# Performance work log

Hardware: AMD Instinct MI355X
Metric: run time of the kernel (lower is better)

Reference implementation:

```python
import jax, jax.numpy as jnp
import numpy as np

K = 8192  # num_embeddings
COMMIT_WEIGHT = 0.25


def setup_inputs() -> dict:
    key = jax.random.key(0)
    k1, k2 = jax.random.split(key)
    B, T, D = 4, 2048, 512
    z = jax.random.normal(k1, (B, T, D), dtype=jnp.float32)
    padding_mask = jnp.zeros((B, T), dtype=bool)  # True = padded; all valid here
    # codebook init: normal(0, dim**-0.5)
    emb = jax.random.normal(k2, (K, D), dtype=jnp.float32) * (D ** -0.5)
    return {"z": z, "padding_mask": padding_mask, "emb": emb}


def reference(z, padding_mask, emb):
    B, T, D = z.shape
    flat = z.reshape(B * T, D)
    dist = (
        jnp.sum(flat * flat, axis=1, keepdims=True)
        - 2.0 * (flat @ emb.T)
        + jnp.sum(emb * emb, axis=1)[None, :]
    )
    indices = jnp.argmin(dist, axis=1)  # [B*T]
    z_q = emb[indices].reshape(B, T, D)
    z_residual = z - jax.lax.stop_gradient(z_q)

    valid = ~padding_mask  # [B, T], True = valid
    vmask = valid.astype(z.dtype)[..., None]  # [B, T, 1]
    n_valid = jnp.maximum(valid.sum(), 1)
    denom = (n_valid * D).astype(z.dtype)

    # commitment: mse(z, sg(z_q)); codebook: mse(z_q, sg(z)) over valid positions
    loss_commit = jnp.sum((z - jax.lax.stop_gradient(z_q)) ** 2 * vmask) / denom
    loss_codebook = jnp.sum((z_q - jax.lax.stop_gradient(z)) ** 2 * vmask) / denom
    vq_loss = loss_codebook + COMMIT_WEIGHT * loss_commit

    # batch stats over valid positions (detached scalars)
    w = valid.reshape(-1).astype(jnp.float32)
    counts = jnp.zeros((K,), dtype=jnp.float32).at[indices].add(w)
    total = jnp.maximum(counts.sum(), 1.0)
    p = counts / total
    entropy = -jnp.sum(p * jnp.log(p + 1e-10))
    perplexity = jnp.exp(entropy)
    codes_used = (counts > 0).sum().astype(jnp.float32)
    codes_used_frac = codes_used / float(K)

    return (z_residual, vq_loss, z_q, perplexity, codes_used, codes_used_frac)
```

## Files before the change

### kernel.cpp

```cpp
#include <hip/hip_runtime.h>
#include <math.h>


#define DDIM 512
#define MTOK 8192
#define KCODE 8192
#define NOUTE (MTOK * DDIM)

#define BM 128
#define BN 128
#define BK 32
#define NK (DDIM / BK)

#define OFF_EH 0u
#define OFF_EL (OFF_EH + (unsigned)KCODE * DDIM * 2u)
#define OFF_ZH (OFF_EL + (unsigned)KCODE * DDIM * 2u)
#define OFF_ZL (OFF_ZH + (unsigned)MTOK * DDIM * 2u)
#define OFF_EE (OFF_ZL + (unsigned)MTOK * DDIM * 2u)
#define OFF_ZZ (OFF_EE + KCODE * 4u)
#define OFF_PACKED (OFF_ZZ + MTOK * 4u)
#define OFF_COUNTS (OFF_PACKED + MTOK * 8u)
#define OFF_SSE (OFF_COUNTS + KCODE * 4u)

typedef _Float16 half8 __attribute__((ext_vector_type(8)));
typedef float f32x16 __attribute__((ext_vector_type(16)));

__global__ __launch_bounds__(256) void prep_kernel(const float* __restrict__ z,
                                                   const float* __restrict__ emb,
                                                   _Float16* __restrict__ eh,
                                                   _Float16* __restrict__ el,
                                                   _Float16* __restrict__ zh,
                                                   _Float16* __restrict__ zl,
                                                   float* __restrict__ zz,
                                                   float* __restrict__ ee) {
  const int row = blockIdx.x * 4 + (threadIdx.x >> 6);
  const int lane = threadIdx.x & 63;
  const float* src;
  _Float16 *dh, *dl;
  float* nrm;
  float sc;
  int r;
  if (row < KCODE) { src = emb + (size_t)row * DDIM; dh = eh; dl = el; nrm = ee; sc = 64.f; r = row; }
  else { src = z + (size_t)(row - KCODE) * DDIM; dh = zh; dl = zl; nrm = zz; sc = 1.f; r = row - KCODE; }
  const float4* s4 = reinterpret_cast<const float4*>(src);
  const float4 v0 = s4[lane * 2 + 0];
  const float4 v1 = s4[lane * 2 + 1];
  const float vv[8] = {v0.x, v0.y, v0.z, v0.w, v1.x, v1.y, v1.z, v1.w};
  half8 hv, lv;
  float s = 0.f;
#pragma unroll
  for (int i = 0; i < 8; ++i) {
    s = fmaf(vv[i], vv[i], s);
    const float vs = vv[i] * sc;
    const _Float16 h = (_Float16)vs;
    hv[i] = h;
    lv[i] = (_Float16)((vs - (float)h) * 2048.0f);
  }
  *reinterpret_cast<half8*>(dh + (size_t)r * DDIM + lane * 8) = hv;
  *reinterpret_cast<half8*>(dl + (size_t)r * DDIM + lane * 8) = lv;
#pragma unroll
  for (int off = 32; off > 0; off >>= 1) s += __shfl_down(s, off, 64);
  if (lane == 0) nrm[r] = s;
}

__device__ __forceinline__ void stage_tile(const char* gb, char* lb) {
#pragma unroll
  for (int i = 0; i < 8; ++i)
    __builtin_amdgcn_global_load_lds(
        (const __attribute__((address_space(1))) unsigned int*)(gb + i * 16384),
        (__attribute__((address_space(3))) unsigned int*)(lb + i * 1024), 16, 0, 0);
}

__global__ __launch_bounds__(256) void argmin_mfma_kernel(
    const _Float16* __restrict__ eh, const _Float16* __restrict__ el,
    const _Float16* __restrict__ zh, const _Float16* __restrict__ zl,
    const float* __restrict__ zz, const float* __restrict__ ee,
    unsigned long long* __restrict__ packed) {
  __shared__ __align__(16) unsigned char smem[65536];

  const int tid = threadIdx.x;
  const int l = tid & 63;
  const int w = tid >> 6;
  const int wr = w >> 1;
  const int wc = w & 1;
  const int codeBase = blockIdx.x * BM;
  const int tokBase = blockIdx.y * BN;

  const _Float16* tileSrc = (w == 0) ? eh + (size_t)codeBase * DDIM
                          : (w == 1) ? el + (size_t)codeBase * DDIM
                          : (w == 2) ? zh + (size_t)tokBase * DDIM
                                     : zl + (size_t)tokBase * DDIM;
  const int cS = (l & 3) ^ ((l >> 3) & 3);
  const char* gsrc = (const char*)tileSrc + (size_t)(l >> 2) * 1024 + cS * 16;
  char* ldsTile = (char*)smem + w * 8192;

  const int keyR = (l >> 1) & 3;
  const int rowA = wr * 64 + (l & 31);
  const int rowB = wc * 64 + (l & 31);
  const int aH = rowA * 64;
  const int aL = 8192 + rowA * 64;
  const int bH = 16384 + rowB * 64;
  const int bL = 24576 + rowB * 64;

  f32x16 hh[2][2], xx[2][2];
#pragma unroll
  for (int mt = 0; mt < 2; ++mt)
#pragma unroll
    for (int nt = 0; nt < 2; ++nt)
#pragma unroll
      for (int i = 0; i < 16; ++i) { hh[mt][nt][i] = 0.f; xx[mt][nt][i] = 0.f; }

#define LDF(off) (*(const half8*)((const char*)smem + (off)))
#define MFMA(a, b, c) __builtin_amdgcn_mfma_f32_32x32x16_f16((a), (b), (c), 0, 0, 0)

  stage_tile(gsrc, ldsTile);
  asm volatile("s_waitcnt vmcnt(0)" ::: "memory");
  __syncthreads();

#pragma unroll 1
  for (int c = 0; c < NK; ++c) {
    const int cur = c & 1;
    if (c + 1 < NK)
      stage_tile(gsrc + (size_t)(c + 1) * 64, ldsTile + (cur ^ 1) * 32768);
    const int bo = cur * 32768;
#pragma unroll
    for (int ks = 0; ks < 2; ++ks) {
      const int cs = ((ks * 2 + (l >> 5)) ^ keyR) << 4;
      const half8 a0h = LDF(bo + aH + cs);
      const half8 a1h = LDF(bo + aH + 2048 + cs);
      const half8 a0l = LDF(bo + aL + cs);
      const half8 a1l = LDF(bo + aL + 2048 + cs);
      const half8 b0h = LDF(bo + bH + cs);
      const half8 b1h = LDF(bo + bH + 2048 + cs);
      const half8 b0l = LDF(bo + bL + cs);
      const half8 b1l = LDF(bo + bL + 2048 + cs);
      hh[0][0] = MFMA(a0h, b0h, hh[0][0]);
      hh[0][1] = MFMA(a0h, b1h, hh[0][1]);
      hh[1][0] = MFMA(a1h, b0h, hh[1][0]);
      hh[1][1] = MFMA(a1h, b1h, hh[1][1]);
      xx[0][0] = MFMA(a0h, b0l, xx[0][0]);
      xx[0][1] = MFMA(a0h, b1l, xx[0][1]);
      xx[1][0] = MFMA(a1h, b0l, xx[1][0]);
      xx[1][1] = MFMA(a1h, b1l, xx[1][1]);
      xx[0][0] = MFMA(a0l, b0h, xx[0][0]);
      xx[0][1] = MFMA(a0l, b1h, xx[0][1]);
      xx[1][0] = MFMA(a1l, b0h, xx[1][0]);
      xx[1][1] = MFMA(a1l, b1h, xx[1][1]);
    }
    asm volatile("s_waitcnt vmcnt(0)" ::: "memory");
    __syncthreads();
  }

  float* eeS = (float*)smem;
  float* pd = (float*)(smem + 512);
  int* pi = (int*)(smem + 1536);
  if (tid < BM) eeS[tid] = ee[codeBase + tid];
  __syncthreads();
#pragma unroll
  for (int nt = 0; nt < 2; ++nt) {
    const int lt = wc * 64 + nt * 32 + (l & 31);
    const float ztt = zz[tokBase + lt];
    float bd = INFINITY;
    int bi = 0x7fffffff;
#pragma unroll
    for (int mt = 0; mt < 2; ++mt)
#pragma unroll
      for (int r = 0; r < 16; ++r) {
        const int rowL = wr * 64 + mt * 32 + (r & 3) + ((r >> 2) << 3) + ((l >> 5) << 2);
        const float dot = hh[mt][nt][r] * (1.0f / 64.0f) + xx[mt][nt][r] * (1.0f / 131072.0f);
        const float dist = (ztt - 2.0f * dot) + eeS[rowL];
        const int code = codeBase + rowL;
        if (dist < bd || (dist == bd && code < bi)) { bd = dist; bi = code; }
      }
    const float od = __shfl_xor(bd, 32, 64);
    const int oi = __shfl_xor(bi, 32, 64);
    if (od < bd || (od == bd && oi < bi)) { bd = od; bi = oi; }
    if (l < 32) { pd[w * 64 + nt * 32 + l] = bd; pi[w * 64 + nt * 32 + l] = bi; }
  }
  __syncthreads();
  if (tid < BN) {
    const int wcc = tid >> 6, rest = tid & 63;
    float da = pd[wcc * 64 + rest];
    int ia = pi[wcc * 64 + rest];
    const float db = pd[(2 + wcc) * 64 + rest];
    const int ib = pi[(2 + wcc) * 64 + rest];
    if (db < da || (db == da && ib < ia)) { da = db; ia = ib; }
    unsigned fb = __float_as_uint(da);
    fb ^= ((unsigned)((int)fb >> 31)) | 0x80000000u;
    const unsigned long long key = ((unsigned long long)fb << 32) | (unsigned)ia;
    atomicMin(&packed[tokBase + tid], key);
  }
#undef LDF
#undef MFMA
}

__global__ __launch_bounds__(256) void gather_kernel(const float* __restrict__ z,
                                                     const float* __restrict__ emb,
                                                     const unsigned long long* __restrict__ packed,
                                                     const unsigned char* __restrict__ mask,
                                                     float* __restrict__ out,
                                                     float* __restrict__ counts,
                                                     double* __restrict__ sse) {
  const int t = blockIdx.x * 4 + (threadIdx.x >> 6);
  const int lane = threadIdx.x & 63;
  const int idx = (int)(packed[t] & 0xffffffffull);
  const float* zp = z + (size_t)t * DDIM;
  const float* ep = emb + (size_t)idx * DDIM;
  float* rp = out + (size_t)t * DDIM;
  float* qp = out + (size_t)NOUTE + 1 + (size_t)t * DDIM;
  float s = 0.f;
#pragma unroll
  for (int j = 0; j < 8; ++j) {
    const int d = j * 64 + lane;
    const float zv = zp[d];
    const float ev = ep[d];
    const float r = zv - ev;
    rp[d] = r;
    qp[d] = ev;
    s = fmaf(r, r, s);
  }
#pragma unroll
  for (int off = 32; off > 0; off >>= 1) s += __shfl_down(s, off, 64);
  if (lane == 0) {
    const float wgt = mask[t] ? 0.0f : 1.0f;
    atomicAdd(sse, (double)s * (double)wgt);
    atomicAdd(&counts[idx], wgt);
  }
}

__global__ __launch_bounds__(1024) void stats_kernel(const float* __restrict__ counts,
                                                     const unsigned char* __restrict__ mask,
                                                     const double* __restrict__ sse,
                                                     float* __restrict__ out) {
  __shared__ double sd[1024];
  __shared__ int si[1024];
  const int tid = threadIdx.x;

  int nv = 0;
  for (int i = tid; i < MTOK; i += 1024) nv += (mask[i] ? 0 : 1);
  si[tid] = nv;
  __syncthreads();
#pragma unroll
  for (int s = 512; s > 0; s >>= 1) {
    if (tid < s) si[tid] += si[tid + s];
    __syncthreads();
  }
  const int n_valid = si[0];
  __syncthreads();

  double ct = 0.0;
  for (int k = tid; k < KCODE; k += 1024) ct += (double)counts[k];
  sd[tid] = ct;
  __syncthreads();
#pragma unroll
  for (int s = 512; s > 0; s >>= 1) {
    if (tid < s) sd[tid] += sd[tid + s];
    __syncthreads();
  }
  const float total = fmaxf((float)sd[0], 1.0f);
  __syncthreads();

  double ent = 0.0;
  int used = 0;
  for (int k = tid; k < KCODE; k += 1024) {
    const float c = counts[k];
    if (c > 0.f) ++used;
    const float p = c / total;
    ent += (double)(p * logf(p + 1e-10f));
  }
  sd[tid] = ent;
  si[tid] = used;
  __syncthreads();
#pragma unroll
  for (int s = 512; s > 0; s >>= 1) {
    if (tid < s) { sd[tid] += sd[tid + s]; si[tid] += si[tid + s]; }
    __syncthreads();
  }
  if (tid == 0) {
    const float entropy = -(float)sd[0];
    const float perp = expf(entropy);
    const int usedc = si[0];
    const int nv1 = n_valid > 1 ? n_valid : 1;
    const float denom = (float)(nv1 * DDIM);
    const float L = (float)sse[0] / denom;
    out[NOUTE] = L + 0.25f * L;
    out[2 * NOUTE + 1] = perp;
    out[2 * NOUTE + 2] = (float)usedc;
    out[2 * NOUTE + 3] = (float)usedc / (float)KCODE;
  }
}

extern "C" void kernel_launch(void* const* d_in, const int* in_sizes, int n_in,
                              void* d_out, int out_size, void* d_ws, size_t ws_size,
                              hipStream_t stream) {
  const float* z = (const float*)d_in[0];
  const unsigned char* mask = (const unsigned char*)d_in[1];
  const float* emb = (const float*)d_in[2];
  float* out = (float*)d_out;
  char* ws = (char*)d_ws;

  _Float16* eh = (_Float16*)(ws + OFF_EH);
  _Float16* el = (_Float16*)(ws + OFF_EL);
  _Float16* zh = (_Float16*)(ws + OFF_ZH);
  _Float16* zl = (_Float16*)(ws + OFF_ZL);
  float* ee = (float*)(ws + OFF_EE);
  float* zz = (float*)(ws + OFF_ZZ);
  unsigned long long* packed = (unsigned long long*)(ws + OFF_PACKED);
  float* counts = (float*)(ws + OFF_COUNTS);
  double* sse = (double*)(ws + OFF_SSE);

  hipMemsetAsync(ws + OFF_PACKED, 0xFF, MTOK * 8u, stream);
  hipMemsetAsync(ws + OFF_COUNTS, 0, KCODE * 4u + 8u, stream);

  hipLaunchKernelGGL(prep_kernel, dim3((KCODE + MTOK) / 4), dim3(256), 0, stream,
                     z, emb, eh, el, zh, zl, zz, ee);
  hipLaunchKernelGGL(argmin_mfma_kernel, dim3(KCODE / BM, MTOK / BN), dim3(256), 0, stream,
                     eh, el, zh, zl, zz, ee, packed);
  hipLaunchKernelGGL(gather_kernel, dim3(MTOK / 4), dim3(256), 0, stream,
                     z, emb, packed, mask, out, counts, sse);
  hipLaunchKernelGGL(stats_kernel, dim3(1), dim3(1024), 0, stream,
                     counts, mask, sse, out);
}
```

Baseline: 436.4 us.

## Replace split-fp16 distance GEMM with single fp16 pass plus bounded fp32 rescue

Drops the hi/lo fp16 split, so the argmin GEMM runs one fp16 MFMA product instead of three and staging traffic is halved. To stay exact, each tile records every code whose approximate distance falls within an error bound (built from the norms) of the running minimum. A new rescue kernel then recomputes those candidates in fp32 and picks the true argmin before gathering. If a token overflows its 128-slot candidate list it falls back to a full fp32 scan over all codes. The cost is extra atomics, candidate writes and per-token fp32 dot products.

After: 597.1 us. +36.8%, slower.

```diff
diff --git a/kernel.cpp b/kernel.cpp
--- a/kernel.cpp
+++ b/kernel.cpp
@@ -11,72 +11,90 @@
 #define BN 128
 #define BK 32
 #define NK (DDIM / BK)
+#define NCAND 128
+#define MARGIN_SLACK 0.02f
 
 #define OFF_EH 0u
-#define OFF_EL (OFF_EH + (unsigned)KCODE * DDIM * 2u)
-#define OFF_ZH (OFF_EL + (unsigned)KCODE * DDIM * 2u)
-#define OFF_ZL (OFF_ZH + (unsigned)MTOK * DDIM * 2u)
-#define OFF_EE (OFF_ZL + (unsigned)MTOK * DDIM * 2u)
+#define OFF_ZH (OFF_EH + (unsigned)KCODE * DDIM * 2u)
+#define OFF_EE (OFF_ZH + (unsigned)MTOK * DDIM * 2u)
 #define OFF_ZZ (OFF_EE + KCODE * 4u)
-#define OFF_PACKED (OFF_ZZ + MTOK * 4u)
-#define OFF_COUNTS (OFF_PACKED + MTOK * 8u)
+#define OFF_SEE (OFF_ZZ + MTOK * 4u)
+#define OFF_SZZ (OFF_SEE + KCODE * 4u)
+#define OFF_PACKED (OFF_SZZ + MTOK * 4u)
+#define OFF_CAND (OFF_PACKED + MTOK * 8u)
+#define OFF_CCNT (OFF_CAND + (unsigned)MTOK * NCAND * 8u)
+#define OFF_COUNTS (OFF_CCNT + MTOK * 4u)
 #define OFF_SSE (OFF_COUNTS + KCODE * 4u)
+#define OFF_SEMAX (OFF_SSE + 8u)
+#define ZERO_BYTES (MTOK * 4u + KCODE * 4u + 8u + 4u)
 
 typedef _Float16 half8 __attribute__((ext_vector_type(8)));
 typedef float f32x16 __attribute__((ext_vector_type(16)));
+
+__device__ __forceinline__ unsigned enc_f(float x) {
+  unsigned u = __float_as_uint(x);
+  return u ^ (((unsigned)((int)u >> 31)) | 0x80000000u);
+}
+__device__ __forceinline__ float dec_f(unsigned y) {
+  return __uint_as_float((y & 0x80000000u) ? (y ^ 0x80000000u) : ~y);
+}
 
 __global__ __launch_bounds__(256) void prep_kernel(const float* __restrict__ z,
                                                    const float* __restrict__ emb,
                                                    _Float16* __restrict__ eh,
-                                                   _Float16* __restrict__ el,
                                                    _Float16* __restrict__ zh,
-                                                   _Float16* __restrict__ zl,
                                                    float* __restrict__ zz,
-                                                   float* __restrict__ ee) {
+                                                   float* __restrict__ ee,
+                                                   float* __restrict__ see,
+                                                   float* __restrict__ szz,
+                                                   unsigned* __restrict__ semax) {
   const int row = blockIdx.x * 4 + (threadIdx.x >> 6);
   const int lane = threadIdx.x & 63;
   const float* src;
-  _Float16 *dh, *dl;
-  float* nrm;
-  float sc;
+  _Float16* dh;
+  float *nrm, *sq;
   int r;
-  if (row < KCODE) { src = emb + (size_t)row * DDIM; dh = eh; dl = el; nrm = ee; sc = 64.f; r = row; }
-  else { src = z + (size_t)(row - KCODE) * DDIM; dh = zh; dl = zl; nrm = zz; sc = 1.f; r = row - KCODE; }
+  bool isEmb;
+  if (row < KCODE) { src = emb + (size_t)row * DDIM; dh = eh; nrm = ee; sq = see; r = row; isEmb = true; }
+  else { src = z + (size_t)(row - KCODE) * DDIM; dh = zh; nrm = zz; sq = szz; r = row - KCODE; isEmb = false; }
   const float4* s4 = reinterpret_cast<const float4*>(src);
   const float4 v0 = s4[lane * 2 + 0];
   const float4 v1 = s4[lane * 2 + 1];
   const float vv[8] = {v0.x, v0.y, v0.z, v0.w, v1.x, v1.y, v1.z, v1.w};
-  half8 hv, lv;
+  half8 hv;
   float s = 0.f;
 #pragma unroll
   for (int i = 0; i < 8; ++i) {
     s = fmaf(vv[i], vv[i], s);
-    const float vs = vv[i] * sc;
-    const _Float16 h = (_Float16)vs;
-    hv[i] = h;
-    lv[i] = (_Float16)((vs - (float)h) * 2048.0f);
+    hv[i] = (_Float16)vv[i];
   }
   *reinterpret_cast<half8*>(dh + (size_t)r * DDIM + lane * 8) = hv;
-  *reinterpret_cast<half8*>(dl + (size_t)r * DDIM + lane * 8) = lv;
 #pragma unroll
   for (int off = 32; off > 0; off >>= 1) s += __shfl_down(s, off, 64);
-  if (lane == 0) nrm[r] = s;
-}
-
-__device__ __forceinline__ void stage_tile(const char* gb, char* lb) {
-#pragma unroll
-  for (int i = 0; i < 8; ++i)
+  if (lane == 0) {
+    nrm[r] = s;
+    const float q = sqrtf(s);
+    sq[r] = q;
+    if (isEmb) atomicMax(semax, enc_f(q));
+  }
+}
+
+__device__ __forceinline__ void stage_half(const char* gb, char* lb) {
+#pragma unroll
+  for (int i = 0; i < 4; ++i)
     __builtin_amdgcn_global_load_lds(
         (const __attribute__((address_space(1))) unsigned int*)(gb + i * 16384),
         (__attribute__((address_space(3))) unsigned int*)(lb + i * 1024), 16, 0, 0);
 }
 
 __global__ __launch_bounds__(256) void argmin_mfma_kernel(
-    const _Float16* __restrict__ eh, const _Float16* __restrict__ el,
-    const _Float16* __restrict__ zh, const _Float16* __restrict__ zl,
+    const _Float16* __restrict__ eh, const _Float16* __restrict__ zh,
     const float* __restrict__ zz, const float* __restrict__ ee,
-    unsigned long long* __restrict__ packed) {
-  __shared__ __align__(16) unsigned char smem[65536];
+    const float* __restrict__ see, const float* __restrict__ szz,
+    const unsigned* __restrict__ semaxp,
+    unsigned long long* __restrict__ packed,
+    int* __restrict__ ccnt, unsigned long long* __restrict__ cand) {
+  __shared__ __align__(16) unsigned char smem[32768];
 
   const int tid = threadIdx.x;
   const int l = tid & 63;
@@ -86,34 +104,30 @@
   const int codeBase = blockIdx.x * BM;
   const int tokBase = blockIdx.y * BN;
 
-  const _Float16* tileSrc = (w == 0) ? eh + (size_t)codeBase * DDIM
-                          : (w == 1) ? el + (size_t)codeBase * DDIM
-                          : (w == 2) ? zh + (size_t)tokBase * DDIM
-                                     : zl + (size_t)tokBase * DDIM;
+  const _Float16* tileSrc = (w < 2) ? eh + (size_t)codeBase * DDIM
+                                    : zh + (size_t)tokBase * DDIM;
   const int cS = (l & 3) ^ ((l >> 3) & 3);
-  const char* gsrc = (const char*)tileSrc + (size_t)(l >> 2) * 1024 + cS * 16;
-  char* ldsTile = (char*)smem + w * 8192;
+  const char* gsrc = (const char*)tileSrc + (size_t)((w & 1) * 64 + (l >> 2)) * 1024 + cS * 16;
+  char* ldsHalf = (char*)smem + (w >> 1) * 8192 + (w & 1) * 4096;
 
   const int keyR = (l >> 1) & 3;
   const int rowA = wr * 64 + (l & 31);
   const int rowB = wc * 64 + (l & 31);
   const int aH = rowA * 64;
-  const int aL = 8192 + rowA * 64;
-  const int bH = 16384 + rowB * 64;
-  const int bL = 24576 + rowB * 64;
-
-  f32x16 hh[2][2], xx[2][2];
+  const int bH = 8192 + rowB * 64;
+
+  f32x16 hh[2][2];
 #pragma unroll
   for (int mt = 0; mt < 2; ++mt)
 #pragma unroll
     for (int nt = 0; nt < 2; ++nt)
 #pragma unroll
-      for (int i = 0; i < 16; ++i) { hh[mt][nt][i] = 0.f; xx[mt][nt][i] = 0.f; }
+      for (int i = 0; i < 16; ++i) hh[mt][nt][i] = 0.f;
 
 #define LDF(off) (*(const half8*)((const char*)smem + (off)))
 #define MFMA(a, b, c) __builtin_amdgcn_mfma_f32_32x32x16_f16((a), (b), (c), 0, 0, 0)
 
-  stage_tile(gsrc, ldsTile);
+  stage_half(gsrc, ldsHalf);
   asm volatile("s_waitcnt vmcnt(0)" ::: "memory");
   __syncthreads();
 
@@ -121,45 +135,38 @@
   for (int c = 0; c < NK; ++c) {
     const int cur = c & 1;
     if (c + 1 < NK)
-      stage_tile(gsrc + (size_t)(c + 1) * 64, ldsTile + (cur ^ 1) * 32768);
-    const int bo = cur * 32768;
+      stage_half(gsrc + (size_t)(c + 1) * 64, ldsHalf + (cur ^ 1) * 16384);
+    const int bo = cur * 16384;
 #pragma unroll
     for (int ks = 0; ks < 2; ++ks) {
       const int cs = ((ks * 2 + (l >> 5)) ^ keyR) << 4;
-      const half8 a0h = LDF(bo + aH + cs);
-      const half8 a1h = LDF(bo + aH + 2048 + cs);
-      const half8 a0l = LDF(bo + aL + cs);
-      const half8 a1l = LDF(bo + aL + 2048 + cs);
-      const half8 b0h = LDF(bo + bH + cs);
-      const half8 b1h = LDF(bo + bH + 2048 + cs);
-      const half8 b0l = LDF(bo + bL + cs);
-      const half8 b1l = LDF(bo + bL + 2048 + cs);
-      hh[0][0] = MFMA(a0h, b0h, hh[0][0]);
-      hh[0][1] = MFMA(a0h, b1h, hh[0][1]);
-      hh[1][0] = MFMA(a1h, b0h, hh[1][0]);
-      hh[1][1] = MFMA(a1h, b1h, hh[1][1]);
-      xx[0][0] = MFMA(a0h, b0l, xx[0][0]);
-      xx[0][1] = MFMA(a0h, b1l, xx[0][1]);
-      xx[1][0] = MFMA(a1h, b0l, xx[1][0]);
-      xx[1][1] = MFMA(a1h, b1l, xx[1][1]);
-      xx[0][0] = MFMA(a0l, b0h, xx[0][0]);
-      xx[0][1] = MFMA(a0l, b1h, xx[0][1]);
-      xx[1][0] = MFMA(a1l, b0h, xx[1][0]);
-      xx[1][1] = MFMA(a1l, b1h, xx[1][1]);
+      const half8 a0 = LDF(bo + aH + cs);
+      const half8 a1 = LDF(bo + aH + 2048 + cs);
+      const half8 b0 = LDF(bo + bH + cs);
+      const half8 b1 = LDF(bo + bH + 2048 + cs);
+      hh[0][0] = MFMA(a0, b0, hh[0][0]);
+      hh[0][1] = MFMA(a0, b1, hh[0][1]);
+      hh[1][0] = MFMA(a1, b0, hh[1][0]);
+      hh[1][1] = MFMA(a1, b1, hh[1][1]);
     }
     asm volatile("s_waitcnt vmcnt(0)" ::: "memory");
     __syncthreads();
   }
 
   float* eeS = (float*)smem;
-  float* pd = (float*)(smem + 512);
-  int* pi = (int*)(smem + 1536);
-  if (tid < BM) eeS[tid] = ee[codeBase + tid];
-  __syncthreads();
+  float* seeS = (float*)(smem + 512);
+  float* pd = (float*)(smem + 1024);
+  int* pi = (int*)(smem + 2048);
+  float* lim = (float*)(smem + 3072);
+  if (tid < BM) { eeS[tid] = ee[codeBase + tid]; seeS[tid] = see[codeBase + tid]; }
+  __syncthreads();
+
+  float ztt[2], szt[2];
 #pragma unroll
   for (int nt = 0; nt < 2; ++nt) {
     const int lt = wc * 64 + nt * 32 + (l & 31);
-    const float ztt = zz[tokBase + lt];
+    ztt[nt] = zz[tokBase + lt];
+    szt[nt] = szz[tokBase + lt];
     float bd = INFINITY;
     int bi = 0x7fffffff;
 #pragma unroll
@@ -167,8 +174,7 @@
 #pragma unroll
       for (int r = 0; r < 16; ++r) {
         const int rowL = wr * 64 + mt * 32 + (r & 3) + ((r >> 2) << 3) + ((l >> 5) << 2);
-        const float dot = hh[mt][nt][r] * (1.0f / 64.0f) + xx[mt][nt][r] * (1.0f / 131072.0f);
-        const float dist = (ztt - 2.0f * dot) + eeS[rowL];
+        const float dist = (ztt[nt] - 2.0f * hh[mt][nt][r]) + eeS[rowL];
         const int code = codeBase + rowL;
         if (dist < bd || (dist == bd && code < bi)) { bd = dist; bi = code; }
       }
@@ -185,46 +191,121 @@
     const float db = pd[(2 + wcc) * 64 + rest];
     const int ib = pi[(2 + wcc) * 64 + rest];
     if (db < da || (db == da && ib < ia)) { da = db; ia = ib; }
-    unsigned fb = __float_as_uint(da);
-    fb ^= ((unsigned)((int)fb >> 31)) | 0x80000000u;
-    const unsigned long long key = ((unsigned long long)fb << 32) | (unsigned)ia;
+    const unsigned long long key = ((unsigned long long)enc_f(da) << 32) | (unsigned)ia;
     atomicMin(&packed[tokBase + tid], key);
+    const unsigned long long curk = packed[tokBase + tid];
+    lim[tid] = fminf(da, dec_f((unsigned)(curk >> 32)));
+  }
+  __syncthreads();
+
+  const float semaxv = dec_f(*semaxp);
+#pragma unroll
+  for (int nt = 0; nt < 2; ++nt) {
+    const int lt = wc * 64 + nt * 32 + (l & 31);
+    const float L = lim[lt];
+    const int tokG = tokBase + lt;
+#pragma unroll
+    for (int mt = 0; mt < 2; ++mt)
+#pragma unroll
+      for (int r = 0; r < 16; ++r) {
+        const int rowL = wr * 64 + mt * 32 + (r & 3) + ((r >> 2) << 3) + ((l >> 5) << 2);
+        const float dist = (ztt[nt] - 2.0f * hh[mt][nt][r]) + eeS[rowL];
+        const float mar = (seeS[rowL] + semaxv) * szt[nt] * (1.0625f / 512.0f) + MARGIN_SLACK;
+        if (dist <= L + mar) {
+          const int pos = atomicAdd(&ccnt[tokG], 1);
+          if (pos < NCAND)
+            cand[(size_t)tokG * NCAND + pos] =
+                ((unsigned long long)enc_f(dist) << 32) | (unsigned)(codeBase + rowL);
+        }
+      }
   }
 #undef LDF
 #undef MFMA
 }
 
-__global__ __launch_bounds__(256) void gather_kernel(const float* __restrict__ z,
-                                                     const float* __restrict__ emb,
-                                                     const unsigned long long* __restrict__ packed,
-                                                     const unsigned char* __restrict__ mask,
-                                                     float* __restrict__ out,
-                                                     float* __restrict__ counts,
-                                                     double* __restrict__ sse) {
+__global__ __launch_bounds__(256) void rescue_gather_kernel(
+    const float* __restrict__ z, const float* __restrict__ emb,
+    const float* __restrict__ zz, const float* __restrict__ ee,
+    const float* __restrict__ see, const float* __restrict__ szz,
+    const unsigned* __restrict__ semaxp,
+    const unsigned long long* __restrict__ packed,
+    const int* __restrict__ ccnt, const unsigned long long* __restrict__ cand,
+    const unsigned char* __restrict__ mask,
+    float* __restrict__ out, float* __restrict__ counts, double* __restrict__ sse) {
   const int t = blockIdx.x * 4 + (threadIdx.x >> 6);
-  const int lane = threadIdx.x & 63;
-  const int idx = (int)(packed[t] & 0xffffffffull);
+  const int l = threadIdx.x & 63;
+  const float zz_t = zz[t];
+  const float szz_t = szz[t];
+  const float semaxv = dec_f(*semaxp);
+  const float M = dec_f((unsigned)(packed[t] >> 32));
   const float* zp = z + (size_t)t * DDIM;
-  const float* ep = emb + (size_t)idx * DDIM;
+  float zv[8];
+#pragma unroll
+  for (int j = 0; j < 8; ++j) zv[j] = zp[j * 64 + l];
+
+  const int n = ccnt[t];
+  float bd = INFINITY;
+  int bi = 0x7fffffff;
+
+  if (n <= NCAND) {
+    for (int base = 0; base < n; base += 64) {
+      const int c = base + l;
+      const bool act = c < n;
+      const unsigned long long key = act ? cand[(size_t)t * NCAND + c] : ~0ull;
+      const int idx = (int)(key & 0xffffffffu);
+      bool keep = false;
+      if (act) {
+        const float dap = dec_f((unsigned)(key >> 32));
+        const float mar = (see[idx] + semaxv) * szz_t * (1.0625f / 512.0f) + MARGIN_SLACK;
+        keep = (dap <= M + mar);
+      }
+      unsigned long long surv = __ballot(keep);
+      while (surv) {
+        const int b = __ffsll(surv) - 1;
+        surv &= surv - 1;
+        const int ci = __shfl(idx, b, 64);
+        const float* ep = emb + (size_t)ci * DDIM;
+        float dot = 0.f;
+#pragma unroll
+        for (int j = 0; j < 8; ++j) dot = fmaf(zv[j], ep[j * 64 + l], dot);
+#pragma unroll
+        for (int off = 32; off > 0; off >>= 1) dot += __shfl_xor(dot, off, 64);
+        const float dx = (zz_t - 2.0f * dot) + ee[ci];
+        if (dx < bd || (dx == bd && ci < bi)) { bd = dx; bi = ci; }
+      }
+    }
+  } else {
+    for (int k = 0; k < KCODE; ++k) {
+      const float* ep = emb + (size_t)k * DDIM;
+      float dot = 0.f;
+#pragma unroll
+      for (int j = 0; j < 8; ++j) dot = fmaf(zv[j], ep[j * 64 + l], dot);
+#pragma unroll
+      for (int off = 32; off > 0; off >>= 1) dot += __shfl_xor(dot, off, 64);
+      const float dx = (zz_t - 2.0f * dot) + ee[k];
+      if (dx < bd || (dx == bd && k < bi)) { bd = dx; bi = k; }
+    }
+  }
+
+  const float* ep = emb + (size_t)bi * DDIM;
   float* rp = out + (size_t)t * DDIM;
   float* qp = out + (size_t)NOUTE + 1 + (size_t)t * DDIM;
   float s = 0.f;
 #pragma unroll
   for (int j = 0; j < 8; ++j) {
-    const int d = j * 64 + lane;
-    const float zv = zp[d];
+    const int d = j * 64 + l;
     const float ev = ep[d];
-    const float r = zv - ev;
+    const float r = zv[j] - ev;
     rp[d] = r;
     qp[d] = ev;
     s = fmaf(r, r, s);
   }
 #pragma unroll
   for (int off = 32; off > 0; off >>= 1) s += __shfl_down(s, off, 64);
-  if (lane == 0) {
+  if (l == 0) {
     const float wgt = mask[t] ? 0.0f : 1.0f;
     atomicAdd(sse, (double)s * (double)wgt);
-    atomicAdd(&counts[idx], wgt);
+    atomicAdd(&counts[bi], wgt);
   }
 }
 
@@ -300,24 +381,28 @@
   char* ws = (char*)d_ws;
 
   _Float16* eh = (_Float16*)(ws + OFF_EH);
-  _Float16* el = (_Float16*)(ws + OFF_EL);
   _Float16* zh = (_Float16*)(ws + OFF_ZH);
-  _Float16* zl = (_Float16*)(ws + OFF_ZL);
   float* ee = (float*)(ws + OFF_EE);
   float* zz = (float*)(ws + OFF_ZZ);
+  float* see = (float*)(ws + OFF_SEE);
+  float* szz = (float*)(ws + OFF_SZZ);
   unsigned long long* packed = (unsigned long long*)(ws + OFF_PACKED);
+  unsigned long long* cand = (unsigned long long*)(ws + OFF_CAND);
+  int* ccnt = (int*)(ws + OFF_CCNT);
   float* counts = (float*)(ws + OFF_COUNTS);
   double* sse = (double*)(ws + OFF_SSE);
+  unsigned* semax = (unsigned*)(ws + OFF_SEMAX);
 
   hipMemsetAsync(ws + OFF_PACKED, 0xFF, MTOK * 8u, stream);
-  hipMemsetAsync(ws + OFF_COUNTS, 0, KCODE * 4u + 8u, stream);
+  hipMemsetAsync(ws + OFF_CCNT, 0, ZERO_BYTES, stream);
 
   hipLaunchKernelGGL(prep_kernel, dim3((KCODE + MTOK) / 4), dim3(256), 0, stream,
-                     z, emb, eh, el, zh, zl, zz, ee);
+                     z, emb, eh, zh, zz, ee, see, szz, semax);
   hipLaunchKernelGGL(argmin_mfma_kernel, dim3(KCODE / BM, MTOK / BN), dim3(256), 0, stream,
-                     eh, el, zh, zl, zz, ee, packed);
-  hipLaunchKernelGGL(gather_kernel, dim3(MTOK / 4), dim3(256), 0, stream,
-                     z, emb, packed, mask, out, counts, sse);
+                     eh, zh, zz, ee, see, szz, semax, packed, ccnt, cand);
+  hipLaunchKernelGGL(rescue_gather_kernel, dim3(MTOK / 4), dim3(256), 0, stream,
+                     z, emb, zz, ee, see, szz, semax, packed, ccnt, cand, mask,
+                     out, counts, sse);
   hipLaunchKernelGGL(stats_kernel, dim3(1), dim3(1024), 0, stream,
                      counts, mask, sse, out);
 }
```
